# Performance work log

Hardware: AMD Instinct MI355X
Metric: run time of the kernel (lower is better)

## Reference

```python
import jax, jax.numpy as jnp
import numpy as np

N_EDGES = 100000
DIM = 64
N_COLS = 8192
PATH_LEN = 256


def setup_inputs() -> dict:
    key = jax.random.key(0)
    k1, k2, k3 = jax.random.split(key, 3)
    x = jax.random.normal(k1, (DIM, N_COLS), dtype=jnp.float32)
    edge_ids = jax.random.randint(k2, (PATH_LEN,), 0, N_EDGES, dtype=jnp.int64)
    # learned parameters (init to small random values instead of torch's zeros
    # so the computation is non-trivial)
    edge_matrix = jax.random.normal(k3, (N_EDGES, DIM, DIM), dtype=jnp.float32) / DIM
    scale = jnp.ones((1,), dtype=jnp.float32)
    return {"x": x, "edge_ids": edge_ids, "edge_matrix": edge_matrix, "scale": scale}


def reference(x, edge_ids, edge_matrix, scale):
    # Sequential recurrence over the edge path:
    #   x <- M[e] @ x + x;  x <- x / ||x||_col
    def step(carry, eid):
        M = edge_matrix[eid]                      # [dim, dim] gather
        y = M @ carry + carry                     # [dim, n_cols]
        y = y / jnp.linalg.norm(y, axis=0, keepdims=True)
        return y, None

    xf, _ = jax.lax.scan(step, x, edge_ids)
    return scale * xf
```

## Files before the change

### kernel.cpp

```cpp
#include <hip/hip_runtime.h>
#include <stdint.h>

#define DIM     64
#define NCOLS   8192
#define CTILE   32
#define SEG     4
#define NLEAF   64
#define NODE    8192
#define MAGIC   0x5A17C0DEu

typedef __attribute__((ext_vector_type(8))) short bfrag8;
typedef __attribute__((ext_vector_type(4))) short bfrag4;
typedef __attribute__((ext_vector_type(4))) float f32x4;

__device__ __forceinline__ unsigned short f2bf(float f) {
  union { float f; unsigned u; } v; v.f = f;
  unsigned r = v.u + 0x7FFFu + ((v.u >> 16) & 1u);
  return (unsigned short)(r >> 16);
}
__device__ __forceinline__ float bf2f(unsigned short h) {
  union { float f; unsigned u; } v; v.u = ((unsigned)h) << 16;
  return v.f;
}
__device__ __forceinline__ float uaf(unsigned u) {
  union { unsigned u; float f; } v; v.u = u; return v.f;
}
__device__ __forceinline__ unsigned cvtpk(float lo, float hi) {
  unsigned r;
  asm("v_cvt_pk_bf16_f32 %0, %1, %2" : "=v"(r) : "v"(lo), "v"(hi));
  return r;
}
__device__ __forceinline__ int swz(int a, int kk) {
  return a * 64 + ((((kk >> 3) ^ a) & 7) << 3) + (kk & 7);
}
__device__ __forceinline__ bfrag8 ldfrag(const unsigned short* P, int a, int ks, int lg) {
  return *(const bfrag8*)&P[swz(a, ks * 32 + lg * 8)];
}
__device__ __forceinline__ void split8(const float* v, bfrag8& H, bfrag8& L) {
  union { bfrag8 f; unsigned u[4]; } h, l;
#pragma unroll
  for (int p = 0; p < 4; ++p) {
    const float a = v[2 * p], c = v[2 * p + 1];
    const unsigned hp = cvtpk(a, c);
    h.u[p] = hp;
    l.u[p] = cvtpk(a - uaf(hp << 16), c - uaf(hp & 0xFFFF0000u));
  }
  H = h.f; L = l.f;
}
__device__ __forceinline__ f32x4 mm3(const bfrag8* aH, const bfrag8* aL,
                                     const bfrag8* bH, const bfrag8* bL) {
  f32x4 acc = {0.f, 0.f, 0.f, 0.f};
#pragma unroll
  for (int ks = 0; ks < 2; ++ks) {
    acc = __builtin_amdgcn_mfma_f32_16x16x32_bf16(aH[ks], bH[ks], acc, 0, 0, 0);
    acc = __builtin_amdgcn_mfma_f32_16x16x32_bf16(aL[ks], bH[ks], acc, 0, 0, 0);
    acc = __builtin_amdgcn_mfma_f32_16x16x32_bf16(aH[ks], bL[ks], acc, 0, 0, 0);
  }
  return acc;
}
__device__ __forceinline__ void wrtile(unsigned short* Sc, int m, int t,
                                       int lg, int lr, f32x4 acc) {
  const int idx = swz(16 * t + lr, 16 * m + 4 * lg);
  union { bfrag4 f; unsigned u[2]; } h, l;
  const unsigned h0 = cvtpk(acc[0], acc[1]);
  const unsigned h1 = cvtpk(acc[2], acc[3]);
  h.u[0] = h0; h.u[1] = h1;
  l.u[0] = cvtpk(acc[0] - uaf(h0 << 16), acc[1] - uaf(h0 & 0xFFFF0000u));
  l.u[1] = cvtpk(acc[2] - uaf(h1 << 16), acc[3] - uaf(h1 & 0xFFFF0000u));
  *(bfrag4*)&Sc[idx]        = h.f;
  *(bfrag4*)&Sc[idx + 4096] = l.f;
}
__device__ void prod1(const unsigned short* Sa, const unsigned short* Sb,
                      unsigned short* Sc, int lane) {
  const int lg = lane >> 4, lr = lane & 15;
  bfrag8 aH[4][2], aL[4][2], bH[4][2], bL[4][2];
#pragma unroll
  for (int m = 0; m < 4; ++m)
#pragma unroll
    for (int ks = 0; ks < 2; ++ks) {
      aH[m][ks] = ldfrag(Sa,        16 * m + lr, ks, lg);
      aL[m][ks] = ldfrag(Sa + 4096, 16 * m + lr, ks, lg);
      bH[m][ks] = ldfrag(Sb,        16 * m + lr, ks, lg);
      bL[m][ks] = ldfrag(Sb + 4096, 16 * m + lr, ks, lg);
    }
#pragma unroll
  for (int m = 0; m < 4; ++m)
#pragma unroll
    for (int t = 0; t < 4; ++t)
      wrtile(Sc, m, t, lg, lr, mm3(aH[m], aL[m], bH[t], bL[t]));
}
__device__ void prod2(const unsigned short* Sa, const unsigned short* Sb,
                      unsigned short* Sc, int lane, int wl) {
  const int lg = lane >> 4, lr = lane & 15;
  bfrag8 aH[2][2], aL[2][2], bH[4][2], bL[4][2];
#pragma unroll
  for (int mm = 0; mm < 2; ++mm)
#pragma unroll
    for (int ks = 0; ks < 2; ++ks) {
      const int m = 2 * wl + mm;
      aH[mm][ks] = ldfrag(Sa,        16 * m + lr, ks, lg);
      aL[mm][ks] = ldfrag(Sa + 4096, 16 * m + lr, ks, lg);
    }
#pragma unroll
  for (int t = 0; t < 4; ++t)
#pragma unroll
    for (int ks = 0; ks < 2; ++ks) {
      bH[t][ks] = ldfrag(Sb,        16 * t + lr, ks, lg);
      bL[t][ks] = ldfrag(Sb + 4096, 16 * t + lr, ks, lg);
    }
#pragma unroll
  for (int mm = 0; mm < 2; ++mm)
#pragma unroll
    for (int t = 0; t < 4; ++t)
      wrtile(Sc, 2 * wl + mm, t, lg, lr, mm3(aH[mm], aL[mm], bH[t], bL[t]));
}
__device__ void prodc(const unsigned short* Sa, const unsigned short* Sb,
                      unsigned short* Sc, int lane, int w) {
  const int lg = lane >> 4, lr = lane & 15;
  bfrag8 aH[2], aL[2], bH[4][2], bL[4][2];
#pragma unroll
  for (int ks = 0; ks < 2; ++ks) {
    aH[ks] = ldfrag(Sa,        16 * w + lr, ks, lg);
    aL[ks] = ldfrag(Sa + 4096, 16 * w + lr, ks, lg);
  }
#pragma unroll
  for (int t = 0; t < 4; ++t)
#pragma unroll
    for (int ks = 0; ks < 2; ++ks) {
      bH[t][ks] = ldfrag(Sb,        16 * t + lr, ks, lg);
      bL[t][ks] = ldfrag(Sb + 4096, 16 * t + lr, ks, lg);
    }
#pragma unroll
  for (int t = 0; t < 4; ++t)
    wrtile(Sc, w, t, lg, lr, mm3(aH, aL, bH[t], bL[t]));
}
__device__ __forceinline__ void export_node(const unsigned short* src,
                                            unsigned short* dst, int tid) {
  const unsigned long long* s = (const unsigned long long*)src;
  unsigned long long* d = (unsigned long long*)dst;
#pragma unroll
  for (int i = 0; i < 8; ++i)
    __hip_atomic_store(&d[tid + i * 256], s[tid + i * 256],
                       __ATOMIC_RELAXED, __HIP_MEMORY_SCOPE_AGENT);
}
__device__ __forceinline__ void waitflag(unsigned int* f) {
  while (__hip_atomic_load(f, __ATOMIC_RELAXED, __HIP_MEMORY_SCOPE_AGENT) != MAGIC)
    __builtin_amdgcn_s_sleep(2);
}
__device__ __forceinline__ void stage_x(const float* __restrict__ x_in, int col0,
                                        int tid, unsigned short* xhiT,
                                        unsigned short* xloT) {
  const int c = tid & 31, g = tid >> 5;
  float v[8];
#pragma unroll
  for (int j = 0; j < 8; ++j)
    v[j] = x_in[(size_t)(8 * g + j) * NCOLS + col0 + c];
  bfrag8 H, L;
  split8(v, H, L);
  const int base = swz(c, 8 * g);
  *(bfrag8*)&xhiT[base] = H;
  *(bfrag8*)&xloT[base] = L;
}

__global__ __launch_bounds__(256) void fused(
    const float* __restrict__ edge_matrix, const int* __restrict__ edge_ids,
    const float* __restrict__ x_in, const float* __restrict__ scale,
    float* __restrict__ out, unsigned short* nodes, unsigned int* flags) {
  __shared__ __align__(16) unsigned short Nd[6][NODE];
  __shared__ __align__(16) unsigned short xhiT[CTILE * 64];
  __shared__ __align__(16) unsigned short xloT[CTILE * 64];
  __shared__ __align__(16) float partial[CTILE * 4];

  const int b = blockIdx.x, tid = threadIdx.x;
  const int lane = tid & 63, w = tid >> 6, lg = lane >> 4, lr = lane & 15;
  unsigned int* flagQ    = flags;
  unsigned int* flagR    = flags + 64;
  unsigned int* flagRoot = flags + 72;
  unsigned short* Rbase = nodes + (size_t)64 * NODE;
  unsigned short* root  = nodes + (size_t)72 * NODE;
  const int col0 = b * CTILE;

  if (b >= NLEAF) stage_x(x_in, col0, tid, xhiT, xloT);

  if (b < NLEAF) {
    const int arow = 16 * w + lr;
    int ids[SEG];
#pragma unroll
    for (int u = 0; u < SEG; ++u) ids[u] = edge_ids[SEG * b + u];
    {
      const float* M0 = edge_matrix + (size_t)ids[0] * 4096;
#pragma unroll
      for (int i = 0; i < 16; ++i) {
        const int e = tid + i * 256;
        const int r = e >> 6, c = e & 63;
        float a = M0[e] + ((r == c) ? 1.0f : 0.0f);
        const unsigned short h = f2bf(a);
        const int idx = swz(c, r);
        Nd[0][idx]        = h;
        Nd[0][idx + 4096] = f2bf(a - bf2f(h));
      }
    }
    f32x4 raw[4], rawn[4];
    {
      const float* Mu = edge_matrix + (size_t)ids[1] * 4096 + (size_t)arow * 64;
#pragma unroll
      for (int ks = 0; ks < 2; ++ks) {
        raw[2 * ks]     = *(const f32x4*)&Mu[ks * 32 + 8 * lg];
        raw[2 * ks + 1] = *(const f32x4*)&Mu[ks * 32 + 8 * lg + 4];
      }
    }
    __syncthreads();

    int cur = 0;
    for (int u = 1; u < SEG; ++u) {
      if (u + 1 < SEG) {
        const float* Mn = edge_matrix + (size_t)ids[u + 1] * 4096 + (size_t)arow * 64;
#pragma unroll
        for (int ks = 0; ks < 2; ++ks) {
          rawn[2 * ks]     = *(const f32x4*)&Mn[ks * 32 + 8 * lg];
          rawn[2 * ks + 1] = *(const f32x4*)&Mn[ks * 32 + 8 * lg + 4];
        }
      }
      bfrag8 aH[2], aL[2];
#pragma unroll
      for (int ks = 0; ks < 2; ++ks) {
        float v[8];
#pragma unroll
        for (int j = 0; j < 8; ++j)
          v[j] = raw[2 * ks + (j >> 2)][j & 3] +
                 ((ks * 32 + 8 * lg + j) == arow ? 1.0f : 0.0f);
        split8(v, aH[ks], aL[ks]);
      }
#pragma unroll
      for (int t = 0; t < 4; ++t) {
        bfrag8 bH[2], bL[2];
#pragma unroll
        for (int ks = 0; ks < 2; ++ks) {
          bH[ks] = ldfrag(Nd[cur],        16 * t + lr, ks, lg);
          bL[ks] = ldfrag(Nd[cur] + 4096, 16 * t + lr, ks, lg);
        }
        wrtile(Nd[cur ^ 1], w, t, lg, lr, mm3(aH, aL, bH, bL));
      }
      __syncthreads();
      cur ^= 1;
#pragma unroll
      for (int q = 0; q < 4; ++q) raw[q] = rawn[q];
    }
    if (b & 1) {
      bfrag8 aH2[2], aL2[2];
#pragma unroll
      for (int ks = 0; ks < 2; ++ks) {
        aH2[ks] = ldfrag(Nd[cur],        16 * w + lr, ks, lg);
        aL2[ks] = ldfrag(Nd[cur] + 4096, 16 * w + lr, ks, lg);
      }
#pragma unroll
      for (int t = 0; t < 4; ++t) {
        bfrag8 ibH[2], ibL[2];
#pragma unroll
        for (int ks = 0; ks < 2; ++ks)
#pragma unroll
          for (int j = 0; j < 8; ++j) {
            ibH[ks][j] = (short)(((16 * t + lr) == (ks * 32 + 8 * lg + j))
                                     ? 0x3F80 : 0);
            ibL[ks][j] = 0;
          }
        wrtile(Nd[2], w, t, lg, lr, mm3(aH2, aL2, ibH, ibL));
      }
      __syncthreads();
    }
    export_node((b & 1) ? Nd[2] : Nd[cur], nodes + (size_t)b * NODE, tid);
    asm volatile("s_waitcnt vmcnt(0)" ::: "memory");
    __syncthreads();
    if (tid == 0)
      __hip_atomic_store(&flagQ[b], MAGIC, __ATOMIC_RELAXED, __HIP_MEMORY_SCOPE_AGENT);
    stage_x(x_in, col0, tid, xhiT, xloT);
  } else if (b <= 72) {
    const bool isC = (b == 72);
    const int g = b - 64;
    const unsigned short* base = isC ? Rbase : nodes + (size_t)(8 * g) * NODE;
    unsigned int* fl = isC ? flagR : &flagQ[8 * g];
    waitflag(&fl[2 * w]);
    waitflag(&fl[2 * w + 1]);
    __builtin_amdgcn_fence(__ATOMIC_ACQUIRE, "agent");
    {
      const unsigned short* Hi = base + (size_t)(2 * w + 1) * NODE;
      const unsigned short* Lo = base + (size_t)(2 * w) * NODE;
      if (w & 1) prod1(Lo, Hi, Nd[w], lane);
      else       prod1(Hi, Lo, Nd[w], lane);
    }
    __syncthreads();
    {
      const int p = w >> 1, wl = w & 1;
      const unsigned short* Hi = Nd[2 * p + 1];
      const unsigned short* Lo = Nd[2 * p];
      if (p & 1) prod2(Lo, Hi, Nd[4 + p], lane, wl);
      else       prod2(Hi, Lo, Nd[4 + p], lane, wl);
    }
    __syncthreads();
    if (isC || (g & 1)) prodc(Nd[4], Nd[5], Nd[0], lane, w);
    else                prodc(Nd[5], Nd[4], Nd[0], lane, w);
    __syncthreads();
    export_node(Nd[0], isC ? root : Rbase + (size_t)g * NODE, tid);
    asm volatile("s_waitcnt vmcnt(0)" ::: "memory");
    __syncthreads();
    if (tid == 0)
      __hip_atomic_store(isC ? flagRoot : &flagR[g], MAGIC,
                         __ATOMIC_RELAXED, __HIP_MEMORY_SCOPE_AGENT);
  }

  if (tid == 0) {
    waitflag(flagRoot);
    __builtin_amdgcn_fence(__ATOMIC_ACQUIRE, "agent");
  }
  __syncthreads();

  const float scl = scale[0];
  bfrag8 aH[2], aL[2];
#pragma unroll
  for (int ks = 0; ks < 2; ++ks) {
    aH[ks] = ldfrag(root,        16 * w + lr, ks, lg);
    aL[ks] = ldfrag(root + 4096, 16 * w + lr, ks, lg);
  }
  f32x4 acc[2];
  float pq[2];
#pragma unroll
  for (int t = 0; t < 2; ++t) {
    const int c = lr + 16 * t;
    bfrag8 bH[2], bL[2];
#pragma unroll
    for (int ks = 0; ks < 2; ++ks) {
      const int idx = swz(c, 32 * ks + 8 * lg);
      bH[ks] = *(const bfrag8*)&xhiT[idx];
      bL[ks] = *(const bfrag8*)&xloT[idx];
    }
    acc[t] = mm3(aH, aL, bH, bL);
    float q = acc[t][0] * acc[t][0] + acc[t][1] * acc[t][1] +
              acc[t][2] * acc[t][2] + acc[t][3] * acc[t][3];
    q += __shfl_xor(q, 16);
    q += __shfl_xor(q, 32);
    pq[t] = q;
  }
  if (lane < 16) {
    partial[(lr +  0) * 4 + w] = pq[0];
    partial[(lr + 16) * 4 + w] = pq[1];
  }
  __syncthreads();
#pragma unroll
  for (int t = 0; t < 2; ++t) {
    const int c = lr + 16 * t;
    f32x4 ps = *(const f32x4*)&partial[c * 4];
    const float inv = scl / sqrtf(ps[0] + ps[1] + ps[2] + ps[3]);
    const size_t rbase = (size_t)(16 * w + 4 * lg) * NCOLS + col0 + c;
    out[rbase]             = acc[t][0] * inv;
    out[rbase + NCOLS]     = acc[t][1] * inv;
    out[rbase + 2 * NCOLS] = acc[t][2] * inv;
    out[rbase + 3 * NCOLS] = acc[t][3] * inv;
  }
}

extern "C" void kernel_launch(void* const* d_in, const int* in_sizes, int n_in,
                              void* d_out, int out_size, void* d_ws, size_t ws_size,
                              hipStream_t stream) {
  const float* x           = (const float*)d_in[0];
  const int*   edge_ids    = (const int*)d_in[1];
  const float* edge_matrix = (const float*)d_in[2];
  const float* scale       = (const float*)d_in[3];
  float* outp              = (float*)d_out;

  unsigned short* nodes = (unsigned short*)d_ws;
  unsigned int*   flags = (unsigned int*)((char*)d_ws + (size_t)73 * NODE * 2);

  fused<<<NCOLS / CTILE, 256, 0, stream>>>(edge_matrix, edge_ids, x, scale,
                                           outp, nodes, flags);
}
```

Before: 15.37 us.

## Halve leaf segment length and add a third level to the product tree

Each leaf block now multiplies two edge matrices instead of four, so 128 leaf blocks feed the tree instead of 64. A new intermediate level of two combiner blocks sits between the 16 R nodes and a single root block (b==146), with new flag and node regions in the workspace. The first matrix is now staged with vectorized bf16 hi/lo split writes instead of scalar stores. This shortens the serial leaf critical path and the leaf load work, but adds one more global-memory handoff and flag wait before the final apply.

```diff
diff --git a/kernel.cpp b/kernel.cpp
--- a/kernel.cpp
+++ b/kernel.cpp
@@ -4,8 +4,8 @@
 #define DIM     64
 #define NCOLS   8192
 #define CTILE   32
-#define SEG     4
-#define NLEAF   64
+#define SEG     2
+#define NLEAF   128
 #define NODE    8192
 #define MAGIC   0x5A17C0DEu
 
@@ -13,15 +13,6 @@
 typedef __attribute__((ext_vector_type(4))) short bfrag4;
 typedef __attribute__((ext_vector_type(4))) float f32x4;
 
-__device__ __forceinline__ unsigned short f2bf(float f) {
-  union { float f; unsigned u; } v; v.f = f;
-  unsigned r = v.u + 0x7FFFu + ((v.u >> 16) & 1u);
-  return (unsigned short)(r >> 16);
-}
-__device__ __forceinline__ float bf2f(unsigned short h) {
-  union { float f; unsigned u; } v; v.u = ((unsigned)h) << 16;
-  return v.f;
-}
 __device__ __forceinline__ float uaf(unsigned u) {
   union { unsigned u; float f; } v; v.u = u; return v.f;
 }
@@ -174,53 +165,50 @@
   const int b = blockIdx.x, tid = threadIdx.x;
   const int lane = tid & 63, w = tid >> 6, lg = lane >> 4, lr = lane & 15;
   unsigned int* flagQ    = flags;
-  unsigned int* flagR    = flags + 64;
-  unsigned int* flagRoot = flags + 72;
-  unsigned short* Rbase = nodes + (size_t)64 * NODE;
-  unsigned short* root  = nodes + (size_t)72 * NODE;
+  unsigned int* flagR    = flags + 128;
+  unsigned int* flagS    = flags + 144;
+  unsigned int* flagRoot = flags + 146;
+  unsigned short* Rbase = nodes + (size_t)128 * NODE;
+  unsigned short* Sbase = nodes + (size_t)144 * NODE;
+  unsigned short* root  = nodes + (size_t)146 * NODE;
   const int col0 = b * CTILE;
 
   if (b >= NLEAF) stage_x(x_in, col0, tid, xhiT, xloT);
 
   if (b < NLEAF) {
     const int arow = 16 * w + lr;
-    int ids[SEG];
-#pragma unroll
-    for (int u = 0; u < SEG; ++u) ids[u] = edge_ids[SEG * b + u];
-    {
-      const float* M0 = edge_matrix + (size_t)ids[0] * 4096;
-#pragma unroll
-      for (int i = 0; i < 16; ++i) {
-        const int e = tid + i * 256;
-        const int r = e >> 6, c = e & 63;
-        float a = M0[e] + ((r == c) ? 1.0f : 0.0f);
-        const unsigned short h = f2bf(a);
-        const int idx = swz(c, r);
-        Nd[0][idx]        = h;
-        Nd[0][idx + 4096] = f2bf(a - bf2f(h));
-      }
-    }
-    f32x4 raw[4], rawn[4];
-    {
-      const float* Mu = edge_matrix + (size_t)ids[1] * 4096 + (size_t)arow * 64;
+    const int id0 = edge_ids[SEG * b], id1 = edge_ids[SEG * b + 1];
+    f32x4 raw[4];
+    {
+      const float* Mu = edge_matrix + (size_t)id1 * 4096 + (size_t)arow * 64;
 #pragma unroll
       for (int ks = 0; ks < 2; ++ks) {
         raw[2 * ks]     = *(const f32x4*)&Mu[ks * 32 + 8 * lg];
         raw[2 * ks + 1] = *(const f32x4*)&Mu[ks * 32 + 8 * lg + 4];
       }
     }
-    __syncthreads();
-
-    int cur = 0;
-    for (int u = 1; u < SEG; ++u) {
-      if (u + 1 < SEG) {
-        const float* Mn = edge_matrix + (size_t)ids[u + 1] * 4096 + (size_t)arow * 64;
-#pragma unroll
-        for (int ks = 0; ks < 2; ++ks) {
-          rawn[2 * ks]     = *(const f32x4*)&Mn[ks * 32 + 8 * lg];
-          rawn[2 * ks + 1] = *(const f32x4*)&Mn[ks * 32 + 8 * lg + 4];
+    {
+      const float* M0 = edge_matrix + (size_t)id0 * 4096;
+      const int c = tid & 63;
+#pragma unroll
+      for (int gg = 0; gg < 2; ++gg) {
+        const int g = 2 * (tid >> 6) + gg;
+        float v[8];
+#pragma unroll
+        for (int j = 0; j < 8; ++j) {
+          const int r = 8 * g + j;
+          v[j] = M0[r * 64 + c] + ((r == c) ? 1.0f : 0.0f);
         }
-      }
+        bfrag8 H, L;
+        split8(v, H, L);
+        const int base = swz(c, 8 * g);
+        *(bfrag8*)&Nd[0][base]        = H;
+        *(bfrag8*)&Nd[0][base + 4096] = L;
+      }
+    }
+    __syncthreads();
+
+    {
       bfrag8 aH[2], aL[2];
 #pragma unroll
       for (int ks = 0; ks < 2; ++ks) {
@@ -236,22 +224,19 @@
         bfrag8 bH[2], bL[2];
 #pragma unroll
         for (int ks = 0; ks < 2; ++ks) {
-          bH[ks] = ldfrag(Nd[cur],        16 * t + lr, ks, lg);
-          bL[ks] = ldfrag(Nd[cur] + 4096, 16 * t + lr, ks, lg);
+          bH[ks] = ldfrag(Nd[0],        16 * t + lr, ks, lg);
+          bL[ks] = ldfrag(Nd[0] + 4096, 16 * t + lr, ks, lg);
         }
-        wrtile(Nd[cur ^ 1], w, t, lg, lr, mm3(aH, aL, bH, bL));
+        wrtile(Nd[1], w, t, lg, lr, mm3(aH, aL, bH, bL));
       }
       __syncthreads();
-      cur ^= 1;
-#pragma unroll
-      for (int q = 0; q < 4; ++q) raw[q] = rawn[q];
     }
     if (b & 1) {
       bfrag8 aH2[2], aL2[2];
 #pragma unroll
       for (int ks = 0; ks < 2; ++ks) {
-        aH2[ks] = ldfrag(Nd[cur],        16 * w + lr, ks, lg);
-        aL2[ks] = ldfrag(Nd[cur] + 4096, 16 * w + lr, ks, lg);
+        aH2[ks] = ldfrag(Nd[1],        16 * w + lr, ks, lg);
+        aL2[ks] = ldfrag(Nd[1] + 4096, 16 * w + lr, ks, lg);
       }
 #pragma unroll
       for (int t = 0; t < 4; ++t) {
@@ -268,17 +253,18 @@
       }
       __syncthreads();
     }
-    export_node((b & 1) ? Nd[2] : Nd[cur], nodes + (size_t)b * NODE, tid);
+    export_node((b & 1) ? Nd[2] : Nd[1], nodes + (size_t)b * NODE, tid);
     asm volatile("s_waitcnt vmcnt(0)" ::: "memory");
     __syncthreads();
     if (tid == 0)
       __hip_atomic_store(&flagQ[b], MAGIC, __ATOMIC_RELAXED, __HIP_MEMORY_SCOPE_AGENT);
     stage_x(x_in, col0, tid, xhiT, xloT);
-  } else if (b <= 72) {
-    const bool isC = (b == 72);
-    const int g = b - 64;
-    const unsigned short* base = isC ? Rbase : nodes + (size_t)(8 * g) * NODE;
-    unsigned int* fl = isC ? flagR : &flagQ[8 * g];
+  } else if (b < 146) {
+    const bool isB = (b >= 144);
+    const int g = b - (isB ? 144 : 128);
+    const unsigned short* base = isB ? Rbase + (size_t)(8 * g) * NODE
+                                     : nodes + (size_t)(8 * g) * NODE;
+    unsigned int* fl = (isB ? flagR : flagQ) + 8 * g;
     waitflag(&fl[2 * w]);
     waitflag(&fl[2 * w + 1]);
     __builtin_amdgcn_fence(__ATOMIC_ACQUIRE, "agent");
@@ -297,15 +283,26 @@
       else       prod2(Hi, Lo, Nd[4 + p], lane, wl);
     }
     __syncthreads();
-    if (isC || (g & 1)) prodc(Nd[4], Nd[5], Nd[0], lane, w);
-    else                prodc(Nd[5], Nd[4], Nd[0], lane, w);
-    __syncthreads();
-    export_node(Nd[0], isC ? root : Rbase + (size_t)g * NODE, tid);
+    if (g & 1) prodc(Nd[4], Nd[5], Nd[0], lane, w);
+    else       prodc(Nd[5], Nd[4], Nd[0], lane, w);
+    __syncthreads();
+    export_node(Nd[0], (isB ? Sbase : Rbase) + (size_t)g * NODE, tid);
     asm volatile("s_waitcnt vmcnt(0)" ::: "memory");
     __syncthreads();
     if (tid == 0)
-      __hip_atomic_store(isC ? flagRoot : &flagR[g], MAGIC,
+      __hip_atomic_store((isB ? flagS : flagR) + g, MAGIC,
                          __ATOMIC_RELAXED, __HIP_MEMORY_SCOPE_AGENT);
+  } else if (b == 146) {
+    waitflag(&flagS[0]);
+    waitflag(&flagS[1]);
+    __builtin_amdgcn_fence(__ATOMIC_ACQUIRE, "agent");
+    prodc(Sbase , Sbase + NODE , Nd[0], lane, w);
+    __syncthreads();
+    export_node(Nd[0], root, tid);
+    asm volatile("s_waitcnt vmcnt(0)" ::: "memory");
+    __syncthreads();
+    if (tid == 0)
+      __hip_atomic_store(flagRoot, MAGIC, __ATOMIC_RELAXED, __HIP_MEMORY_SCOPE_AGENT);
   }
 
   if (tid == 0) {
@@ -368,7 +365,7 @@
   float* outp              = (float*)d_out;
 
   unsigned short* nodes = (unsigned short*)d_ws;
-  unsigned int*   flags = (unsigned int*)((char*)d_ws + (size_t)73 * NODE * 2);
+  unsigned int*   flags = (unsigned int*)((char*)d_ws + (size_t)147 * NODE * 2);
 
   fused<<<NCOLS / CTILE, 256, 0, stream>>>(edge_matrix, edge_ids, x, scale,
                                            outp, nodes, flags);
```

After: 15.96 us. +3.8%, slower.

## Tree-reduce leaf segment products and write final tiles directly to global

Applied to the files above, without the earlier changes.

Leaf blocks now stage three edge matrices at once and form their 4-matrix product as a two-level tree: two waves multiply M1 by M0 while the other two multiply M2 by M3. The previous version ran three dependent serial products followed by an extra identity-multiply transpose pass for odd blocks. The final product in both leaf and interior blocks is written straight to global memory with atomic stores, removing the LDS staging step and the separate export copy with its barrier. This shortens the critical path of the scan tree. The cost is more LDS staging work up front and uncoalesced global writes of fragment tiles. prod1 is also restructured to lower register pressure.

```diff
diff --git a/kernel.cpp b/kernel.cpp
--- a/kernel.cpp
+++ b/kernel.cpp
@@ -4,7 +4,6 @@
 #define DIM     64
 #define NCOLS   8192
 #define CTILE   32
-#define SEG     4
 #define NLEAF   64
 #define NODE    8192
 #define MAGIC   0x5A17C0DEu
@@ -13,15 +12,6 @@
 typedef __attribute__((ext_vector_type(4))) short bfrag4;
 typedef __attribute__((ext_vector_type(4))) float f32x4;
 
-__device__ __forceinline__ unsigned short f2bf(float f) {
-  union { float f; unsigned u; } v; v.f = f;
-  unsigned r = v.u + 0x7FFFu + ((v.u >> 16) & 1u);
-  return (unsigned short)(r >> 16);
-}
-__device__ __forceinline__ float bf2f(unsigned short h) {
-  union { float f; unsigned u; } v; v.u = ((unsigned)h) << 16;
-  return v.f;
-}
 __device__ __forceinline__ float uaf(unsigned u) {
   union { unsigned u; float f; } v; v.u = u; return v.f;
 }
@@ -70,24 +60,43 @@
   *(bfrag4*)&Sc[idx]        = h.f;
   *(bfrag4*)&Sc[idx + 4096] = l.f;
 }
+__device__ __forceinline__ void wrtileG(unsigned short* Sc, int m, int t,
+                                        int lg, int lr, f32x4 acc) {
+  const int idx = swz(16 * t + lr, 16 * m + 4 * lg);
+  union { unsigned u[2]; unsigned long long q; } h, l;
+  const unsigned h0 = cvtpk(acc[0], acc[1]);
+  const unsigned h1 = cvtpk(acc[2], acc[3]);
+  h.u[0] = h0; h.u[1] = h1;
+  l.u[0] = cvtpk(acc[0] - uaf(h0 << 16), acc[1] - uaf(h0 & 0xFFFF0000u));
+  l.u[1] = cvtpk(acc[2] - uaf(h1 << 16), acc[3] - uaf(h1 & 0xFFFF0000u));
+  __hip_atomic_store((unsigned long long*)&Sc[idx], h.q,
+                     __ATOMIC_RELAXED, __HIP_MEMORY_SCOPE_AGENT);
+  __hip_atomic_store((unsigned long long*)&Sc[idx + 4096], l.q,
+                     __ATOMIC_RELAXED, __HIP_MEMORY_SCOPE_AGENT);
+}
 __device__ void prod1(const unsigned short* Sa, const unsigned short* Sb,
                       unsigned short* Sc, int lane) {
   const int lg = lane >> 4, lr = lane & 15;
-  bfrag8 aH[4][2], aL[4][2], bH[4][2], bL[4][2];
-#pragma unroll
-  for (int m = 0; m < 4; ++m)
-#pragma unroll
-    for (int ks = 0; ks < 2; ++ks) {
-      aH[m][ks] = ldfrag(Sa,        16 * m + lr, ks, lg);
-      aL[m][ks] = ldfrag(Sa + 4096, 16 * m + lr, ks, lg);
-      bH[m][ks] = ldfrag(Sb,        16 * m + lr, ks, lg);
-      bL[m][ks] = ldfrag(Sb + 4096, 16 * m + lr, ks, lg);
-    }
-#pragma unroll
-  for (int m = 0; m < 4; ++m)
+  bfrag8 bH[4][2], bL[4][2];
+#pragma unroll
+  for (int t = 0; t < 4; ++t)
+#pragma unroll
+    for (int ks = 0; ks < 2; ++ks) {
+      bH[t][ks] = ldfrag(Sb,        16 * t + lr, ks, lg);
+      bL[t][ks] = ldfrag(Sb + 4096, 16 * t + lr, ks, lg);
+    }
+#pragma unroll
+  for (int m = 0; m < 4; ++m) {
+    bfrag8 aH[2], aL[2];
+#pragma unroll
+    for (int ks = 0; ks < 2; ++ks) {
+      aH[ks] = ldfrag(Sa,        16 * m + lr, ks, lg);
+      aL[ks] = ldfrag(Sa + 4096, 16 * m + lr, ks, lg);
+    }
 #pragma unroll
     for (int t = 0; t < 4; ++t)
-      wrtile(Sc, m, t, lg, lr, mm3(aH[m], aL[m], bH[t], bL[t]));
+      wrtile(Sc, m, t, lg, lr, mm3(aH, aL, bH[t], bL[t]));
+  }
 }
 __device__ void prod2(const unsigned short* Sa, const unsigned short* Sb,
                       unsigned short* Sc, int lane, int wl) {
@@ -114,8 +123,8 @@
     for (int t = 0; t < 4; ++t)
       wrtile(Sc, 2 * wl + mm, t, lg, lr, mm3(aH[mm], aL[mm], bH[t], bL[t]));
 }
-__device__ void prodc(const unsigned short* Sa, const unsigned short* Sb,
-                      unsigned short* Sc, int lane, int w) {
+__device__ void prodcG(const unsigned short* Sa, const unsigned short* Sb,
+                       unsigned short* Sc, int lane, int w) {
   const int lg = lane >> 4, lr = lane & 15;
   bfrag8 aH[2], aL[2], bH[4][2], bL[4][2];
 #pragma unroll
@@ -132,16 +141,7 @@
     }
 #pragma unroll
   for (int t = 0; t < 4; ++t)
-    wrtile(Sc, w, t, lg, lr, mm3(aH, aL, bH[t], bL[t]));
-}
-__device__ __forceinline__ void export_node(const unsigned short* src,
-                                            unsigned short* dst, int tid) {
-  const unsigned long long* s = (const unsigned long long*)src;
-  unsigned long long* d = (unsigned long long*)dst;
-#pragma unroll
-  for (int i = 0; i < 8; ++i)
-    __hip_atomic_store(&d[tid + i * 256], s[tid + i * 256],
-                       __ATOMIC_RELAXED, __HIP_MEMORY_SCOPE_AGENT);
+    wrtileG(Sc, w, t, lg, lr, mm3(aH, aL, bH[t], bL[t]));
 }
 __device__ __forceinline__ void waitflag(unsigned int* f) {
   while (__hip_atomic_load(f, __ATOMIC_RELAXED, __HIP_MEMORY_SCOPE_AGENT) != MAGIC)
@@ -183,92 +183,90 @@
   if (b >= NLEAF) stage_x(x_in, col0, tid, xhiT, xloT);
 
   if (b < NLEAF) {
-    const int arow = 16 * w + lr;
-    int ids[SEG];
-#pragma unroll
-    for (int u = 0; u < SEG; ++u) ids[u] = edge_ids[SEG * b + u];
+    const int* eb = edge_ids + 4 * b;
+    const int id0 = eb[0], id1 = eb[1], id2 = eb[2], id3 = eb[3];
+
+    f32x4 raw[2][4];
+    if (w < 2) {
+      const float* M1 = edge_matrix + (size_t)id1 * 4096;
+#pragma unroll
+      for (int mm = 0; mm < 2; ++mm) {
+        const float* Mr = M1 + (size_t)(16 * (2 * w + mm) + lr) * 64;
+#pragma unroll
+        for (int ks = 0; ks < 2; ++ks) {
+          raw[mm][2 * ks]     = *(const f32x4*)&Mr[ks * 32 + 8 * lg];
+          raw[mm][2 * ks + 1] = *(const f32x4*)&Mr[ks * 32 + 8 * lg + 4];
+        }
+      }
+    }
     {
-      const float* M0 = edge_matrix + (size_t)ids[0] * 4096;
-#pragma unroll
-      for (int i = 0; i < 16; ++i) {
-        const int e = tid + i * 256;
-        const int r = e >> 6, c = e & 63;
-        float a = M0[e] + ((r == c) ? 1.0f : 0.0f);
-        const unsigned short h = f2bf(a);
-        const int idx = swz(c, r);
-        Nd[0][idx]        = h;
-        Nd[0][idx + 4096] = f2bf(a - bf2f(h));
+      const int c = tid & 63;
+      const float* M0 = edge_matrix + (size_t)id0 * 4096;
+      const float* M2 = edge_matrix + (size_t)id2 * 4096;
+      const float* M3 = edge_matrix + (size_t)id3 * 4096;
+#pragma unroll
+      for (int gg = 0; gg < 2; ++gg) {
+        const int g = 2 * w + gg;
+        float v0[8], v2[8], v3[8];
+#pragma unroll
+        for (int j = 0; j < 8; ++j) {
+          const int r = 8 * g + j;
+          const float d = (r == c) ? 1.0f : 0.0f;
+          v0[j] = M0[r * 64 + c] + d;
+          v2[j] = M2[r * 64 + c] + d;
+        }
+        const f32x4 u0 = *(const f32x4*)&M3[c * 64 + 8 * g];
+        const f32x4 u1 = *(const f32x4*)&M3[c * 64 + 8 * g + 4];
+#pragma unroll
+        for (int j = 0; j < 8; ++j) {
+          const int k = 8 * g + j;
+          v3[j] = (j < 4 ? u0[j] : u1[j - 4]) + ((c == k) ? 1.0f : 0.0f);
+        }
+        bfrag8 H, L;
+        const int base = swz(c, 8 * g);
+        split8(v0, H, L);
+        *(bfrag8*)&Nd[0][base] = H;  *(bfrag8*)&Nd[0][base + 4096] = L;
+        split8(v2, H, L);
+        *(bfrag8*)&Nd[1][base] = H;  *(bfrag8*)&Nd[1][base + 4096] = L;
+        split8(v3, H, L);
+        *(bfrag8*)&Nd[2][base] = H;  *(bfrag8*)&Nd[2][base + 4096] = L;
       }
     }
-    f32x4 raw[4], rawn[4];
-    {
-      const float* Mu = edge_matrix + (size_t)ids[1] * 4096 + (size_t)arow * 64;
-#pragma unroll
-      for (int ks = 0; ks < 2; ++ks) {
-        raw[2 * ks]     = *(const f32x4*)&Mu[ks * 32 + 8 * lg];
-        raw[2 * ks + 1] = *(const f32x4*)&Mu[ks * 32 + 8 * lg + 4];
+    __syncthreads();
+
+    if (w < 2) {
+#pragma unroll
+      for (int mm = 0; mm < 2; ++mm) {
+        const int arow = 16 * (2 * w + mm) + lr;
+        bfrag8 aH[2], aL[2];
+#pragma unroll
+        for (int ks = 0; ks < 2; ++ks) {
+          float v[8];
+#pragma unroll
+          for (int j = 0; j < 8; ++j)
+            v[j] = raw[mm][2 * ks + (j >> 2)][j & 3] +
+                   ((ks * 32 + 8 * lg + j) == arow ? 1.0f : 0.0f);
+          split8(v, aH[ks], aL[ks]);
+        }
+#pragma unroll
+        for (int t = 0; t < 4; ++t) {
+          bfrag8 bH[2], bL[2];
+#pragma unroll
+          for (int ks = 0; ks < 2; ++ks) {
+            bH[ks] = ldfrag(Nd[0],        16 * t + lr, ks, lg);
+            bL[ks] = ldfrag(Nd[0] + 4096, 16 * t + lr, ks, lg);
+          }
+          wrtile(Nd[3], 2 * w + mm, t, lg, lr, mm3(aH, aL, bH, bL));
+        }
       }
-    }
-    __syncthreads();
-
-    int cur = 0;
-    for (int u = 1; u < SEG; ++u) {
-      if (u + 1 < SEG) {
-        const float* Mn = edge_matrix + (size_t)ids[u + 1] * 4096 + (size_t)arow * 64;
-#pragma unroll
-        for (int ks = 0; ks < 2; ++ks) {
-          rawn[2 * ks]     = *(const f32x4*)&Mn[ks * 32 + 8 * lg];
-          rawn[2 * ks + 1] = *(const f32x4*)&Mn[ks * 32 + 8 * lg + 4];
-        }
-      }
-      bfrag8 aH[2], aL[2];
-#pragma unroll
-      for (int ks = 0; ks < 2; ++ks) {
-        float v[8];
-#pragma unroll
-        for (int j = 0; j < 8; ++j)
-          v[j] = raw[2 * ks + (j >> 2)][j & 3] +
-                 ((ks * 32 + 8 * lg + j) == arow ? 1.0f : 0.0f);
-        split8(v, aH[ks], aL[ks]);
-      }
-#pragma unroll
-      for (int t = 0; t < 4; ++t) {
-        bfrag8 bH[2], bL[2];
-#pragma unroll
-        for (int ks = 0; ks < 2; ++ks) {
-          bH[ks] = ldfrag(Nd[cur],        16 * t + lr, ks, lg);
-          bL[ks] = ldfrag(Nd[cur] + 4096, 16 * t + lr, ks, lg);
-        }
-        wrtile(Nd[cur ^ 1], w, t, lg, lr, mm3(aH, aL, bH, bL));
-      }
-      __syncthreads();
-      cur ^= 1;
-#pragma unroll
-      for (int q = 0; q < 4; ++q) raw[q] = rawn[q];
-    }
-    if (b & 1) {
-      bfrag8 aH2[2], aL2[2];
-#pragma unroll
-      for (int ks = 0; ks < 2; ++ks) {
-        aH2[ks] = ldfrag(Nd[cur],        16 * w + lr, ks, lg);
-        aL2[ks] = ldfrag(Nd[cur] + 4096, 16 * w + lr, ks, lg);
-      }
-#pragma unroll
-      for (int t = 0; t < 4; ++t) {
-        bfrag8 ibH[2], ibL[2];
-#pragma unroll
-        for (int ks = 0; ks < 2; ++ks)
-#pragma unroll
-          for (int j = 0; j < 8; ++j) {
-            ibH[ks][j] = (short)(((16 * t + lr) == (ks * 32 + 8 * lg + j))
-                                     ? 0x3F80 : 0);
-            ibL[ks][j] = 0;
-          }
-        wrtile(Nd[2], w, t, lg, lr, mm3(aH2, aL2, ibH, ibL));
-      }
-      __syncthreads();
-    }
-    export_node((b & 1) ? Nd[2] : Nd[cur], nodes + (size_t)b * NODE, tid);
+    } else {
+      prod2(Nd[1], Nd[2], Nd[4], lane, w - 2);
+    }
+    __syncthreads();
+
+    unsigned short* qslot = nodes + (size_t)b * NODE;
+    if (b & 1) prodcG(Nd[3], Nd[4], qslot, lane, w);
+    else       prodcG(Nd[4], Nd[3], qslot, lane, w);
     asm volatile("s_waitcnt vmcnt(0)" ::: "memory");
     __syncthreads();
     if (tid == 0)
@@ -297,10 +295,9 @@
       else       prod2(Hi, Lo, Nd[4 + p], lane, wl);
     }
     __syncthreads();
-    if (isC || (g & 1)) prodc(Nd[4], Nd[5], Nd[0], lane, w);
-    else                prodc(Nd[5], Nd[4], Nd[0], lane, w);
-    __syncthreads();
-    export_node(Nd[0], isC ? root : Rbase + (size_t)g * NODE, tid);
+    unsigned short* dst = isC ? root : Rbase + (size_t)g * NODE;
+    if (isC || (g & 1)) prodcG(Nd[4], Nd[5], dst, lane, w);
+    else                prodcG(Nd[5], Nd[4], dst, lane, w);
     asm volatile("s_waitcnt vmcnt(0)" ::: "memory");
     __syncthreads();
     if (tid == 0)
```

New measurement: 16.04 us. 4.4% more time.
